# Kernel optimization log

Hardware: AMD Instinct MI355X
Metric: run time of the kernel (lower is better)

The kernel has to match this reference:

```python
import jax, jax.numpy as jnp
import numpy as np

DIM = 2048
NUM_HEADS = 16
NUM_KV_HEADS = 4
HEAD_DIM = DIM // NUM_HEADS  # 128
ROPE_DIMS = HEAD_DIM         # rope_dims=0 -> full head_dim
ROPE_BASE = 10000.0
EPS = jnp.finfo(jnp.float32).eps  # torch F.rms_norm default eps


def _rms_norm(x):
    # F.rms_norm over last dim, no learned weight
    return x * jax.lax.rsqrt(jnp.mean(x * x, axis=-1, keepdims=True) + EPS)


def _rope_cos_sin(seq_len, dtype):
    inv_freq = 1.0 / (ROPE_BASE ** (jnp.arange(0, ROPE_DIMS, 2, dtype=jnp.float32) / ROPE_DIMS))
    t = jnp.arange(seq_len, dtype=jnp.float32)
    freqs = jnp.outer(t, inv_freq)  # [S, rope_dims/2]
    return jnp.cos(freqs).astype(dtype), jnp.sin(freqs).astype(dtype)


def _apply_rotary(x, cos, sin):
    # x: [B, H, S, hd]; cos/sin: [S, rope_dims/2] broadcast over B,H
    half = ROPE_DIMS // 2
    x1, x2 = x[..., :half], x[..., half:ROPE_DIMS]
    x_pass = x[..., ROPE_DIMS:]
    rotated = jnp.concatenate((x1 * cos + x2 * sin, -x1 * sin + x2 * cos), axis=-1)
    return jnp.concatenate((rotated, x_pass), axis=-1) if x_pass.shape[-1] else rotated


def setup_inputs() -> dict:
    key = jax.random.key(0)
    ks = jax.random.split(key, 6)
    B, S = 2, 2048
    kv_dim = NUM_KV_HEADS * HEAD_DIM
    scale = 0.02
    return {
        "x": jax.random.normal(ks[0], (B, S, DIM), dtype=jnp.float32),
        "Wq": jax.random.normal(ks[1], (DIM, DIM), dtype=jnp.float32) * scale,
        "Wk": jax.random.normal(ks[2], (kv_dim, DIM), dtype=jnp.float32) * scale,
        "Wv": jax.random.normal(ks[3], (kv_dim, DIM), dtype=jnp.float32) * scale,
        "Wproj": jax.random.normal(ks[4], (DIM, DIM), dtype=jnp.float32) * scale,
        "q_gain": jnp.full((NUM_HEADS,), 1.0, dtype=jnp.float32),
    }


def reference(x, Wq, Wk, Wv, Wproj, q_gain):
    B, S, D = x.shape
    H, KV, hd = NUM_HEADS, NUM_KV_HEADS, HEAD_DIM
    group = H // KV

    # QKV projections (Linear: y = x @ W.T)
    q = (x @ Wq.T).reshape(B, S, H, hd).transpose(0, 2, 1, 3)    # [B,H,S,hd]
    k = (x @ Wk.T).reshape(B, S, KV, hd).transpose(0, 2, 1, 3)   # [B,KV,S,hd]
    v = (x @ Wv.T).reshape(B, S, KV, hd).transpose(0, 2, 1, 3)

    # Per-head RMSNorm on q/k
    q = _rms_norm(q)
    k = _rms_norm(k)

    # RoPE
    cos, sin = _rope_cos_sin(S, q.dtype)
    q = _apply_rotary(q, cos, sin)
    k = _apply_rotary(k, cos, sin)

    # Per-head gain on q
    q = q * q_gain[None, :, None, None]

    # GQA: expand kv heads to H
    k = jnp.repeat(k, group, axis=1)  # [B,H,S,hd]
    v = jnp.repeat(v, group, axis=1)

    # Causal SDPA
    sm_scale = 1.0 / np.sqrt(hd)
    scores = jnp.einsum('bhqd,bhkd->bhqk', q, k) * sm_scale
    causal = jnp.tril(jnp.ones((S, S), dtype=bool))
    scores = jnp.where(causal, scores, -jnp.inf)
    attn = jax.nn.softmax(scores, axis=-1)
    y = jnp.einsum('bhqk,bhkd->bhqd', attn, v)

    y = y.transpose(0, 2, 1, 3).reshape(B, S, D)
    return y @ Wproj.T
```

## Files before the change

### kernel.cpp

```cpp
#include <hip/hip_runtime.h>
#include <hip/hip_bf16.h>
#include <stdint.h>

namespace {

constexpr int kB = 2;
constexpr int kS = 2048;
constexpr int kD = 2048;
constexpr int kH = 16;
constexpr int kKV = 4;
constexpr int kHd = 128;
constexpr int kM = kB * kS;
constexpr int kQKN = kD + kKV * kHd;

using bf = __bf16;
typedef bf bf16x8 __attribute__((ext_vector_type(8)));
typedef float f32x4 __attribute__((ext_vector_type(4)));
typedef float f32x16 __attribute__((ext_vector_type(16)));

__device__ __forceinline__ f32x4 mfma16(bf16x8 a, bf16x8 b, f32x4 c) {
  return __builtin_amdgcn_mfma_f32_16x16x32_bf16(a, b, c, 0, 0, 0);
}
__device__ __forceinline__ f32x16 mfma32(bf16x8 a, bf16x8 b, f32x16 c) {
  return __builtin_amdgcn_mfma_f32_32x32x16_bf16(a, b, c, 0, 0, 0);
}

__device__ __forceinline__ void gload_lds16(const bf* g, bf* l) {
  __builtin_amdgcn_global_load_lds(
      (const __attribute__((address_space(1))) void*)(uintptr_t)g,
      (__attribute__((address_space(3))) void*)l, 16, 0, 0);
}

__global__ __launch_bounds__(256) void cvt_all(
    const float* __restrict__ x, const float* __restrict__ wq,
    const float* __restrict__ wk, const float* __restrict__ wv,
    const float* __restrict__ wp, bf* __restrict__ xb,
    bf* __restrict__ wqkvb, bf* __restrict__ wpb) {
  int i = blockIdx.x * 256 + threadIdx.x;
  const float* src; bf* dst; int off;
  if (i < 2097152)      { src = x;  dst = xb;    off = i; }
  else if (i < 3145728) { src = wq; dst = wqkvb; off = i - 2097152; }
  else if (i < 3407872) { src = wk; dst = wqkvb + (size_t)kD * kD;               off = i - 3145728; }
  else if (i < 3670016) { src = wv; dst = wqkvb + (size_t)kD * kD + 512 * kD;    off = i - 3407872; }
  else                  { src = wp; dst = wpb;   off = i - 3670016; }
  float4 v = reinterpret_cast<const float4*>(src)[off];
  union { bf h[4]; uint2 u; } o;
  o.h[0] = (bf)v.x; o.h[1] = (bf)v.y; o.h[2] = (bf)v.z; o.h[3] = (bf)v.w;
  reinterpret_cast<uint2*>(dst)[off] = o.u;
}

template <typename CT, int TM>
__device__ __forceinline__ void gemm_body(const bf* __restrict__ A, int lda,
                                          const bf* __restrict__ Bm, int ldb,
                                          CT* __restrict__ C, int ldc, int K,
                                          int bx, int by, bf* As, bf* Bs) {
  const int tid = threadIdx.x;
  const int w = tid >> 6, lane = tid & 63;
  const int r16 = lane & 15, kg = lane >> 4;
  const int bm = by * TM, bn = bx * 128;
  const int wy = (w >> 1) * (TM / 2), wx = (w & 1) * 64;
  constexpr int MF = TM / 32;
  f32x4 acc[MF][4] = {};
  for (int kt = 0; kt < K; kt += 64) {
    __syncthreads();
#pragma unroll
    for (int r = 0; r < MF; r++) {
      int u = r * 256 + tid;
      int row = u >> 3;
      int cb = ((u & 7) * 16) ^ ((row & 7) << 4);
      gload_lds16(A + (size_t)(bm + row) * lda + kt + (cb >> 1),
                  As + (size_t)(r * 256 + w * 64) * 8);
    }
#pragma unroll
    for (int r = 0; r < 4; r++) {
      int u = r * 256 + tid;
      int row = u >> 3;
      int cb = ((u & 7) * 16) ^ ((row & 7) << 4);
      gload_lds16(Bm + (size_t)(bn + row) * ldb + kt + (cb >> 1),
                  Bs + (size_t)(r * 256 + w * 64) * 8);
    }
    __syncthreads();
#pragma unroll
    for (int ks = 0; ks < 2; ks++) {
      bf16x8 af[MF], bfr[4];
#pragma unroll
      for (int m = 0; m < MF; m++) {
        int row = wy + m * 16 + r16;
        af[m] = *reinterpret_cast<const bf16x8*>(
            reinterpret_cast<const char*>(As) + row * 128 +
            ((ks * 64 + kg * 16) ^ ((row & 7) << 4)));
      }
#pragma unroll
      for (int n = 0; n < 4; n++) {
        int row = wx + n * 16 + r16;
        bfr[n] = *reinterpret_cast<const bf16x8*>(
            reinterpret_cast<const char*>(Bs) + row * 128 +
            ((ks * 64 + kg * 16) ^ ((row & 7) << 4)));
      }
#pragma unroll
      for (int m = 0; m < MF; m++)
#pragma unroll
        for (int n = 0; n < 4; n++)
          acc[m][n] = mfma16(af[m], bfr[n], acc[m][n]);
    }
  }
#pragma unroll
  for (int m = 0; m < MF; m++)
#pragma unroll
    for (int n = 0; n < 4; n++)
#pragma unroll
      for (int r = 0; r < 4; r++) {
        int row = bm + wy + m * 16 + kg * 4 + r;
        int col = bn + wx + n * 16 + r16;
        C[(size_t)row * ldc + col] = (CT)acc[m][n][r];
      }
}

__global__ __launch_bounds__(256) void gemm_qkv_vt(
    const bf* __restrict__ xb, const bf* __restrict__ wqkb,
    bf* __restrict__ qkbuf, const bf* __restrict__ wvb,
    bf* __restrict__ vtbuf) {
  __shared__ bf As[128 * 64];
  __shared__ bf Bs[128 * 64];
  const int bid = blockIdx.x;
  if (bid < 640) {
    int xcd = bid & 7, i = bid >> 3;
    int cx = xcd & 1, cy = xcd >> 1;
    int bx = cx * 10 + i % 10;
    int by = cy * 8 + i / 10;
    gemm_body<bf, 128>(xb, kD, wqkb, kD, qkbuf, kQKN, kD, bx, by, As, Bs);
  } else {
    int b2 = bid - 640;
    int xcd = b2 & 7, i = b2 >> 3;
    int bx = xcd * 4 + i % 4;
    int by = i / 4;
    gemm_body<bf, 64>(wvb, kD, xb, kD, vtbuf, kM, kD, bx, by, As, Bs);
  }
}

__global__ __launch_bounds__(256) void gemm_proj(const bf* __restrict__ yb,
                                                 const bf* __restrict__ wpb,
                                                 float* __restrict__ out) {
  __shared__ bf As[128 * 64];
  __shared__ bf Bs[128 * 64];
  const int bid = blockIdx.x;
  int xcd = bid & 7, i = bid >> 3;
  int cx = xcd & 1, cy = xcd >> 1;
  int bx = cx * 8 + i % 8;
  int by = cy * 8 + i / 8;
  gemm_body<float, 128>(yb, kD, wpb, kD, out, kD, kD, bx, by, As, Bs);
}

__global__ __launch_bounds__(256) void normrope(bf* __restrict__ qk,
                                                const float* __restrict__ qgain) {
  const int tid = threadIdx.x;
  const int w = tid >> 6, lane = tid & 63;
  int v = blockIdx.x * 4 + w;
  int b = v / (kS * (kH + kKV));
  int rem = v % (kS * (kH + kKV));
  int s = rem / (kH + kKV);
  int j = rem % (kH + kKV);
  int colbase = (j < kH) ? j * kHd : kD + (j - kH) * kHd;
  size_t base = (size_t)(b * kS + s) * kQKN + colbase;
  float e1 = (float)qk[base + lane];
  float e2 = (float)qk[base + 64 + lane];
  float ss = e1 * e1 + e2 * e2;
#pragma unroll
  for (int m = 1; m < 64; m <<= 1) ss += __shfl_xor(ss, m);
  float inv = rsqrtf(ss * (1.0f / 128.0f) + 1.1920929e-7f);
  e1 *= inv; e2 *= inv;
  float invfreq = exp2f((float)lane * -0.20762050593046013f);
  float ang = (float)s * invfreq;
  float sn, cs;
  sincosf(ang, &sn, &cs);
  float o1 = e1 * cs + e2 * sn;
  float o2 = -e1 * sn + e2 * cs;
  if (j < kH) {
    float g = qgain[j] * (0.08838834764831845f * 1.4426950408889634f);
    o1 *= g; o2 *= g;
  }
  qk[base + lane] = (bf)o1;
  qk[base + 64 + lane] = (bf)o2;
}

__global__ __launch_bounds__(256, 2) void attn_kernel(const bf* __restrict__ qk,
                                                      const bf* __restrict__ vt,
                                                      bf* __restrict__ y) {
  __shared__ bf Ks[2][64 * 128];
  __shared__ bf Vs[2][128 * 64];
  __shared__ float Ml[2][64][2];
  const int tid = threadIdx.x;
  const int w = tid >> 6, lane = tid & 63;
  const int q32 = lane & 31, hi = lane >> 5;
  const int qhalf = w & 1, kvhalf = w >> 1;
  const int bh = blockIdx.x;
  const int pairIdx = blockIdx.y;
  const int b = bh >> 4, h = bh & 15, kvh = h >> 2;
  const size_t rowbase = (size_t)b * kS;
  const bf* kbase = qk + kD + kvh * kHd;
  const bf* vbase = vt + (size_t)(kvh * kHd) * kM + b * kS;

  const bf* gK[4]; const bf* gV[4];
#pragma unroll
  for (int r = 0; r < 4; r++) {
    int u = r * 256 + tid;
    int krow = u >> 4, c16 = u & 15;
    gK[r] = kbase + (size_t)(rowbase + krow) * kQKN +
            (((c16 * 16) ^ ((krow & 7) << 4)) >> 1);
    int vrow = u >> 3, c8 = u & 7;
    gV[r] = vbase + (size_t)vrow * kM +
            (((c8 * 16) ^ ((vrow & 7) << 4)) >> 1);
  }

  auto stage = [&](int buf, int kt) {
    const size_t ko = (size_t)kt * (size_t)(64 * kQKN);
    const int vo = kt * 64;
#pragma unroll
    for (int r = 0; r < 4; r++)
      gload_lds16(gK[r] + ko, Ks[buf] + (size_t)(r * 256 + w * 64) * 8);
#pragma unroll
    for (int r = 0; r < 4; r++)
      gload_lds16(gV[r] + vo, Vs[buf] + (size_t)(r * 256 + w * 64) * 8);
  };

#pragma unroll 1
  for (int ph = 0; ph < 2; ph++) {
    const int j = ph ? (31 - pairIdx) : pairIdx;
    const int q0 = j * 64;
    const int qg0 = q0 + qhalf * 32;
    const int qrow = qg0 + q32;
    const int kvoff = kvhalf * 32;

    bf16x8 qf[8];
#pragma unroll
    for (int dc = 0; dc < 8; dc++)
      qf[dc] = *reinterpret_cast<const bf16x8*>(
          qk + (rowbase + qrow) * kQKN + h * kHd + dc * 16 + hi * 8);

    f32x16 o[4] = {};
    float mrun = -1e30f, lrun = 0.f;

    int cur = 0;
    stage(0, 0);

    for (int kt = 0; kt <= j; kt++) {
      asm volatile("s_barrier" ::: "memory");
      if (kt < j) {
        stage(cur ^ 1, kt + 1);
        asm volatile("s_waitcnt vmcnt(8)" ::: "memory");
      } else {
        asm volatile("s_waitcnt vmcnt(0)" ::: "memory");
      }
      asm volatile("s_barrier" ::: "memory");

      if (kt * 64 + kvoff <= qg0 + 31) {
        f32x16 sf = {};
        const int krow = kvoff + q32;
        const char* ksrow = reinterpret_cast<const char*>(Ks[cur]) + krow * 256;
        const int kswz = (krow & 7) << 4;
        __builtin_amdgcn_s_setprio(1);
#pragma unroll
        for (int dc = 0; dc < 8; dc++) {
          bf16x8 kf = *reinterpret_cast<const bf16x8*>(
              ksrow + ((dc * 32 + hi * 16) ^ kswz));
          sf = mfma32(kf, qf[dc], sf);
        }
        __builtin_amdgcn_s_setprio(0);

        if (kt * 64 + kvoff + 31 > qg0) {
#pragma unroll
          for (int r = 0; r < 16; r++) {
            int kgl = kt * 64 + kvoff + (r & 3) + 8 * (r >> 2) + 4 * hi;
            sf[r] = (kgl <= qrow) ? sf[r] : -1e30f;
          }
        }

        float rmax = sf[0];
#pragma unroll
        for (int r = 1; r < 16; r++) rmax = fmaxf(rmax, sf[r]);
        rmax = fmaxf(rmax, __shfl_xor(rmax, 32));

        if (!__all(rmax <= mrun + 8.0f)) {
          float mnew = fmaxf(mrun, rmax);
          float resc = exp2f(mrun - mnew);
          mrun = mnew;
          lrun *= resc;
          float rq[16];
#pragma unroll
          for (int r = 0; r < 16; r++)
            rq[r] = __shfl(resc, (r & 3) + 8 * (r >> 2) + 4 * hi);
#pragma unroll
          for (int db = 0; db < 4; db++)
#pragma unroll
            for (int r = 0; r < 16; r++) o[db][r] *= rq[r];
        }

        float rsum = 0.f;
#pragma unroll
        for (int r = 0; r < 16; r++) {
          float p = exp2f(sf[r] - mrun);
          sf[r] = p;
          rsum += p;
        }
        rsum += __shfl_xor(rsum, 32);
        lrun += rsum;

        bf16x8 pa[2];
        {
          uint32_t wa[4], wb[4];
#pragma unroll
          for (int g = 0; g < 4; g++) {
            asm("v_cvt_pk_bf16_f32 %0, %1, %2"
                : "=v"(wa[g]) : "v"(sf[4 * g + 0]), "v"(sf[4 * g + 1]));
            asm("v_cvt_pk_bf16_f32 %0, %1, %2"
                : "=v"(wb[g]) : "v"(sf[4 * g + 2]), "v"(sf[4 * g + 3]));
          }
          asm volatile("v_permlane32_swap_b32 %0, %1" : "+v"(wa[0]), "+v"(wa[1]));
          asm volatile("v_permlane32_swap_b32 %0, %1" : "+v"(wb[0]), "+v"(wb[1]));
          asm volatile("v_permlane32_swap_b32 %0, %1" : "+v"(wa[2]), "+v"(wa[3]));
          asm volatile("v_permlane32_swap_b32 %0, %1" : "+v"(wb[2]), "+v"(wb[3]));
          union { uint32_t u[4]; bf16x8 v; } p0, p1;
          p0.u[0] = wa[0]; p0.u[1] = wb[0]; p0.u[2] = wa[1]; p0.u[3] = wb[1];
          p1.u[0] = wa[2]; p1.u[1] = wb[2]; p1.u[2] = wa[3]; p1.u[3] = wb[3];
          pa[0] = p0.v; pa[1] = p1.v;
        }

        __builtin_amdgcn_s_setprio(1);
#pragma unroll
        for (int c = 0; c < 2; c++)
#pragma unroll
          for (int db = 0; db < 4; db++) {
            int vrow = db * 32 + q32;
            bf16x8 vb = *reinterpret_cast<const bf16x8*>(
                reinterpret_cast<const char*>(Vs[cur]) + vrow * 128 +
                ((kvhalf * 64 + c * 32 + hi * 16) ^ ((vrow & 7) << 4)));
            o[db] = mfma32(pa[c], vb, o[db]);
          }
        __builtin_amdgcn_s_setprio(0);
      }
      cur ^= 1;
    }

    __syncthreads();
    float* mb = reinterpret_cast<float*>(Ks);
    if (w >= 2) {
      Ml[w - 2][lane][0] = mrun;
      Ml[w - 2][lane][1] = lrun;
      int base = (w - 2) * 4096;
#pragma unroll
      for (int db = 0; db < 4; db++)
#pragma unroll
        for (int r = 0; r < 16; r++)
          mb[base + (db * 16 + r) * 64 + lane] = o[db][r];
    }
    __syncthreads();
    if (w < 2) {
      float m1 = Ml[w][lane][0], l1 = Ml[w][lane][1];
      float m = fmaxf(mrun, m1);
      float f0 = exp2f(mrun - m), f1 = exp2f(m1 - m);
      float linv = 1.0f / (lrun * f0 + l1 * f1);
      float av = f0 * linv, bv = f1 * linv;
      float aq[16], bq[16];
#pragma unroll
      for (int r = 0; r < 16; r++) {
        int cr = (r & 3) + 8 * (r >> 2) + 4 * hi;
        aq[r] = __shfl(av, cr);
        bq[r] = __shfl(bv, cr);
      }
      int base = w * 4096;
#pragma unroll
      for (int db = 0; db < 4; db++)
#pragma unroll
        for (int r = 0; r < 16; r++) {
          float pv = mb[base + (db * 16 + r) * 64 + lane];
          float res = o[db][r] * aq[r] + pv * bq[r];
          int s = qg0 + (r & 3) + 8 * (r >> 2) + 4 * hi;
          int d = db * 32 + q32;
          y[(rowbase + s) * kD + h * kHd + d] = (bf)res;
        }
    }
    __syncthreads();
  }
}

}

extern "C" void kernel_launch(void* const* d_in, const int* in_sizes, int n_in,
                              void* d_out, int out_size, void* d_ws, size_t ws_size,
                              hipStream_t stream) {
  const float* x  = (const float*)d_in[0];
  const float* Wq = (const float*)d_in[1];
  const float* Wk = (const float*)d_in[2];
  const float* Wv = (const float*)d_in[3];
  const float* Wp = (const float*)d_in[4];
  const float* qg = (const float*)d_in[5];

  bf* xb    = (bf*)d_ws;
  bf* wqkvb = xb + (size_t)kM * kD;
  bf* wpb   = wqkvb + (size_t)3072 * kD;
  bf* qkbuf = wpb + (size_t)kD * kD;
  bf* vtbuf = qkbuf + (size_t)kM * kQKN;
  bf* yb    = vtbuf + (size_t)512 * kM;

  cvt_all<<<18432, 256, 0, stream>>>(x, Wq, Wk, Wv, Wp, xb, wqkvb, wpb);

  gemm_qkv_vt<<<896, 256, 0, stream>>>(
      xb, wqkvb, qkbuf, wqkvb + (size_t)(kD + 512) * kD, vtbuf);

  normrope<<<(kB * kS * (kH + kKV)) / 4, 256, 0, stream>>>(qkbuf, qg);

  attn_kernel<<<dim3(kB * kH, 16), 256, 0, stream>>>(qkbuf, vtbuf, yb);

  gemm_proj<<<512, 256, 0, stream>>>(yb, wpb, (float*)d_out);
}
```

Baseline: 216.5 us.

## Fuse per-head RMSNorm, RoPE and q gain into the QKV GEMM epilogue

```diff
diff --git a/kernel.cpp b/kernel.cpp
--- a/kernel.cpp
+++ b/kernel.cpp
@@ -49,11 +49,12 @@
   reinterpret_cast<uint2*>(dst)[off] = o.u;
 }
 
-template <typename CT, int TM>
+template <typename CT, int TM, bool NR = false>
 __device__ __forceinline__ void gemm_body(const bf* __restrict__ A, int lda,
                                           const bf* __restrict__ Bm, int ldb,
                                           CT* __restrict__ C, int ldc, int K,
-                                          int bx, int by, bf* As, bf* Bs) {
+                                          int bx, int by, bf* As, bf* Bs,
+                                          float* ssb, const float* qgain) {
   const int tid = threadIdx.x;
   const int w = tid >> 6, lane = tid & 63;
   const int r16 = lane & 15, kg = lane >> 4;
@@ -104,37 +105,119 @@
           acc[m][n] = mfma16(af[m], bfr[n], acc[m][n]);
     }
   }
-#pragma unroll
-  for (int m = 0; m < MF; m++)
-#pragma unroll
-    for (int n = 0; n < 4; n++)
-#pragma unroll
-      for (int r = 0; r < 4; r++) {
-        int row = bm + wy + m * 16 + kg * 4 + r;
-        int col = bn + wx + n * 16 + r16;
-        C[(size_t)row * ldc + col] = (CT)acc[m][n][r];
-      }
+
+  if constexpr (!NR) {
+#pragma unroll
+    for (int m = 0; m < MF; m++)
+#pragma unroll
+      for (int n = 0; n < 4; n++)
+#pragma unroll
+        for (int r = 0; r < 4; r++) {
+          int row = bm + wy + m * 16 + kg * 4 + r;
+          int col = bn + wx + n * 16 + r16;
+          C[(size_t)row * ldc + col] = (CT)acc[m][n][r];
+        }
+  } else {
+    __syncthreads();
+    const int wxbit = (wx != 0);
+    float rmsi[MF][4];
+    {
+      float ssv[MF][4];
+#pragma unroll
+      for (int m = 0; m < MF; m++)
+#pragma unroll
+        for (int r = 0; r < 4; r++) {
+          float s2 = 0.f;
+#pragma unroll
+          for (int n = 0; n < 4; n++) { float v = acc[m][n][r]; s2 += v * v; }
+          s2 += __shfl_xor(s2, 1);
+          s2 += __shfl_xor(s2, 2);
+          s2 += __shfl_xor(s2, 4);
+          s2 += __shfl_xor(s2, 8);
+          ssv[m][r] = s2;
+        }
+      if (r16 == 0) {
+#pragma unroll
+        for (int m = 0; m < MF; m++)
+#pragma unroll
+          for (int r = 0; r < 4; r++)
+            ssb[(wy + m * 16 + kg * 4 + r) * 2 + wxbit] = ssv[m][r];
+      }
+      __syncthreads();
+#pragma unroll
+      for (int m = 0; m < MF; m++)
+#pragma unroll
+        for (int r = 0; r < 4; r++) {
+          int row = wy + m * 16 + kg * 4 + r;
+          float tot = ssb[row * 2 + 0] + ssb[row * 2 + 1];
+          rmsi[m][r] = rsqrtf(tot * (1.0f / 128.0f) + 1.1920929e-7f);
+        }
+    }
+#pragma unroll
+    for (int m = 0; m < MF; m++)
+#pragma unroll
+      for (int n = 0; n < 4; n++)
+#pragma unroll
+        for (int r = 0; r < 4; r++) {
+          int row = wy + m * 16 + kg * 4 + r;
+          int col = wx + n * 16 + r16;
+          int byte = (row * 256 + col * 2) ^ ((row & 7) << 4);
+          *reinterpret_cast<bf*>(reinterpret_cast<char*>(As) + byte) =
+              (bf)(acc[m][n][r] * rmsi[m][r]);
+        }
+    __syncthreads();
+    const int head = bn >> 7;
+    const bool isq = bn < kD;
+    const float g = isq
+        ? qgain[head] * (0.08838834764831845f * 1.4426950408889634f)
+        : 1.0f;
+#pragma unroll
+    for (int m = 0; m < MF; m++)
+#pragma unroll
+      for (int n = 0; n < 4; n++) {
+        int fi = n * 16 + r16;
+        float invf = exp2f((float)fi * -0.20762050593046013f);
+#pragma unroll
+        for (int r = 0; r < 4; r++) {
+          int row = wy + m * 16 + kg * 4 + r;
+          int srow = (bm + row) & (kS - 1);
+          float sn, cs;
+          sincosf((float)srow * invf, &sn, &cs);
+          int pcol = (wx ^ 64) + n * 16 + r16;
+          int pbyte = (row * 256 + pcol * 2) ^ ((row & 7) << 4);
+          float pv = (float)*reinterpret_cast<const bf*>(
+              reinterpret_cast<const char*>(As) + pbyte);
+          float own = acc[m][n][r] * rmsi[m][r];
+          float out = wxbit ? (own * cs - pv * sn)
+                            : (own * cs + pv * sn);
+          C[(size_t)(bm + row) * ldc + (bn + wx + n * 16 + r16)] =
+              (CT)(out * g);
+        }
+      }
+  }
 }
 
 __global__ __launch_bounds__(256) void gemm_qkv_vt(
     const bf* __restrict__ xb, const bf* __restrict__ wqkb,
     bf* __restrict__ qkbuf, const bf* __restrict__ wvb,
-    bf* __restrict__ vtbuf) {
-  __shared__ bf As[128 * 64];
-  __shared__ bf Bs[128 * 64];
+    bf* __restrict__ vtbuf, const float* __restrict__ qg) {
+  __shared__ bf SH[2][128 * 64];
+  __shared__ float ssb[128 * 2];
   const int bid = blockIdx.x;
   if (bid < 640) {
     int xcd = bid & 7, i = bid >> 3;
     int cx = xcd & 1, cy = xcd >> 1;
     int bx = cx * 10 + i % 10;
     int by = cy * 8 + i / 10;
-    gemm_body<bf, 128>(xb, kD, wqkb, kD, qkbuf, kQKN, kD, bx, by, As, Bs);
+    gemm_body<bf, 128, true>(xb, kD, wqkb, kD, qkbuf, kQKN, kD,
+                             bx, by, SH[0], SH[1], ssb, qg);
   } else {
     int b2 = bid - 640;
     int xcd = b2 & 7, i = b2 >> 3;
     int bx = xcd * 4 + i % 4;
     int by = i / 4;
-    gemm_body<bf, 64>(wvb, kD, xb, kD, vtbuf, kM, kD, bx, by, As, Bs);
+    gemm_body<bf, 64>(wvb, kD, xb, kD, vtbuf, kM, kD,
+                      bx, by, SH[0], SH[1], nullptr, nullptr);
   }
 }
 
@@ -148,39 +231,8 @@
   int cx = xcd & 1, cy = xcd >> 1;
   int bx = cx * 8 + i % 8;
   int by = cy * 8 + i / 8;
-  gemm_body<float, 128>(yb, kD, wpb, kD, out, kD, kD, bx, by, As, Bs);
-}
-
-__global__ __launch_bounds__(256) void normrope(bf* __restrict__ qk,
-                                                const float* __restrict__ qgain) {
-  const int tid = threadIdx.x;
-  const int w = tid >> 6, lane = tid & 63;
-  int v = blockIdx.x * 4 + w;
-  int b = v / (kS * (kH + kKV));
-  int rem = v % (kS * (kH + kKV));
-  int s = rem / (kH + kKV);
-  int j = rem % (kH + kKV);
-  int colbase = (j < kH) ? j * kHd : kD + (j - kH) * kHd;
-  size_t base = (size_t)(b * kS + s) * kQKN + colbase;
-  float e1 = (float)qk[base + lane];
-  float e2 = (float)qk[base + 64 + lane];
-  float ss = e1 * e1 + e2 * e2;
-#pragma unroll
-  for (int m = 1; m < 64; m <<= 1) ss += __shfl_xor(ss, m);
-  float inv = rsqrtf(ss * (1.0f / 128.0f) + 1.1920929e-7f);
-  e1 *= inv; e2 *= inv;
-  float invfreq = exp2f((float)lane * -0.20762050593046013f);
-  float ang = (float)s * invfreq;
-  float sn, cs;
-  sincosf(ang, &sn, &cs);
-  float o1 = e1 * cs + e2 * sn;
-  float o2 = -e1 * sn + e2 * cs;
-  if (j < kH) {
-    float g = qgain[j] * (0.08838834764831845f * 1.4426950408889634f);
-    o1 *= g; o2 *= g;
-  }
-  qk[base + lane] = (bf)o1;
-  qk[base + 64 + lane] = (bf)o2;
+  gemm_body<float, 128>(yb, kD, wpb, kD, out, kD, kD, bx, by, As, Bs,
+                        nullptr, nullptr);
 }
 
 __global__ __launch_bounds__(256, 2) void attn_kernel(const bf* __restrict__ qk,
@@ -405,9 +457,7 @@
   cvt_all<<<18432, 256, 0, stream>>>(x, Wq, Wk, Wv, Wp, xb, wqkvb, wpb);
 
   gemm_qkv_vt<<<896, 256, 0, stream>>>(
-      xb, wqkvb, qkbuf, wqkvb + (size_t)(kD + 512) * kD, vtbuf);
-
-  normrope<<<(kB * kS * (kH + kKV)) / 4, 256, 0, stream>>>(qkbuf, qg);
+      xb, wqkvb, qkbuf, wqkvb + (size_t)(kD + 512) * kD, vtbuf, qg);
 
   attn_kernel<<<dim3(kB * kH, 16), 256, 0, stream>>>(qkbuf, vtbuf, yb);
 
```

New measurement: 533.6 us. 146% more time.
